# Kernel tuning notes

Measured on AMD Instinct MI355X. Metric: run time of the kernel, lower is better.

Reference implementation:

```python
import jax, jax.numpy as jnp
import numpy as np

DIM = 256
HEADS = 8
DIM_HEAD = 64
INNER = HEADS * DIM_HEAD  # 512
B, H, W = 4, 128, 128


def setup_inputs() -> dict:
    key = jax.random.key(0)
    ks = jax.random.split(key, 7)
    x = jax.random.normal(ks[0], (B, DIM, H, W), dtype=jnp.float32)
    context = jax.random.normal(ks[1], (B, DIM, H, W), dtype=jnp.float32)
    # weights stored as (in, out) so projection is x @ W
    s_in = 1.0 / np.sqrt(DIM)
    s_inner = 1.0 / np.sqrt(INNER)
    Wq = jax.random.uniform(ks[2], (DIM, INNER), jnp.float32, -s_in, s_in)
    Wk = jax.random.uniform(ks[3], (DIM, INNER), jnp.float32, -s_in, s_in)
    Wv = jax.random.uniform(ks[4], (DIM, INNER), jnp.float32, -s_in, s_in)
    Wo = jax.random.uniform(ks[5], (INNER, DIM), jnp.float32, -s_inner, s_inner)
    bo = jax.random.uniform(ks[6], (DIM,), jnp.float32, -s_inner, s_inner)
    return {"x": x, "context": context, "Wq": Wq, "Wk": Wk, "Wv": Wv, "Wo": Wo, "bo": bo}


def reference(x, context, Wq, Wk, Wv, Wo, bo):
    b, c, h, w = x.shape
    n = h * w
    x_flat = x.reshape(b, c, n).transpose(0, 2, 1)          # b n c
    ctx_flat = context.reshape(b, c, n).transpose(0, 2, 1)  # b n c
    # projections; split heads: b n (h d) -> b h n d
    def heads(t):
        return t.reshape(b, n, HEADS, DIM_HEAD).transpose(0, 2, 1, 3)
    q = heads(x_flat @ Wq)
    k = heads(ctx_flat @ Wk)
    v = heads(ctx_flat @ Wv)
    # column-wise softmax over token dim n (axis=-2). NOTE: original module
    # defines scale but never applies it, so we faithfully omit it.
    k = jax.nn.softmax(k, axis=-2)
    cm = jnp.einsum('bhnd,bhne->bhde', k, v)   # small d x e context matrix
    out = jnp.einsum('bhnd,bhde->bhne', q, cm)  # b h n e
    out = out.transpose(0, 2, 1, 3).reshape(b, n, INNER)
    out = out @ Wo + bo
    out = out.transpose(0, 2, 1).reshape(b, c, h, w)
    return x + out
```

## Files before the change

### kernel.cpp

```cpp
#include <hip/hip_runtime.h>

typedef unsigned short u16;
typedef u16   u16x4  __attribute__((ext_vector_type(4)));
typedef u16   u16x8  __attribute__((ext_vector_type(8)));
typedef __bf16 bf16x8 __attribute__((ext_vector_type(8)));
typedef float f32x4  __attribute__((ext_vector_type(4)));

constexpr int BATCH  = 4;
constexpr int CDIM   = 256;
constexpr int NTOK   = 16384;
constexpr int INNERD = 512;

__device__ __forceinline__ u16 f2b(float f) {
  return __builtin_bit_cast(u16, (__bf16)f);
}
__device__ __forceinline__ float b2f(u16 b) {
  return (float)__builtin_bit_cast(__bf16, b);
}

__device__ __forceinline__ void async_ld16(const u16* g, u16* l) {
  __builtin_amdgcn_global_load_lds(
      (const __attribute__((address_space(1))) void*)g,
      (__attribute__((address_space(3))) void*)l, 16, 0, 0);
}

constexpr int ZERO_N = BATCH * 8 * 64 * 64 + BATCH * INNERD;
__global__ __launch_bounds__(256) void prep(
    const float* __restrict__ x, const float* __restrict__ ctx,
    const float* __restrict__ Wk, const float* __restrict__ Wv,
    u16* __restrict__ xt, u16* __restrict__ ct,
    u16* __restrict__ kt, u16* __restrict__ vt,
    float* __restrict__ zbuf) {
  __shared__ float tile[64][33];
  int id = blockIdx.x;
  if (id < 16384) {
    int bx = id & 511, by = (id >> 9) & 3, zb = id >> 11;
    int b = zb >> 1;
    const float* src = (zb & 1) ? ctx : x;
    u16* dst = (zb & 1) ? ct : xt;
    src += (size_t)b * CDIM * NTOK;
    dst += (size_t)b * NTOK * CDIM;
    int n0 = bx * 32, c0 = by * 64;
    int tx = threadIdx.x & 31, ty = threadIdx.x >> 5;
#pragma unroll
    for (int i = 0; i < 64; i += 8)
      tile[ty + i][tx] = src[(size_t)(c0 + ty + i) * NTOK + n0 + tx];
    __syncthreads();
    int nl = threadIdx.x >> 3;
    int cl = (threadIdx.x & 7) * 8;
    u16x8 o;
#pragma unroll
    for (int j = 0; j < 8; j++) o[j] = f2b(tile[cl + j][nl]);
    *(u16x8*)&dst[(size_t)(n0 + nl) * CDIM + c0 + cl] = o;
  } else if (id < 16640) {
    int idw = id - 16384;
    int bx = idw & 15, by = (idw >> 4) & 7, bz = idw >> 7;
    float (*t2)[33] = (float(*)[33])tile;
    const float* src = bz == 0 ? Wk : Wv;
    u16* dst = bz == 0 ? kt : vt;
    int i0 = bx * 32, c0 = by * 32;
    int tx = threadIdx.x & 31, ty = threadIdx.x >> 5;
#pragma unroll
    for (int r = 0; r < 32; r += 8)
      t2[ty + r][tx] = src[(size_t)(c0 + ty + r) * INNERD + i0 + tx];
    __syncthreads();
#pragma unroll
    for (int r = 0; r < 32; r += 8)
      dst[(size_t)(i0 + ty + r) * CDIM + c0 + tx] = f2b(t2[tx][ty + r]);
  } else {
    int i = (id - 16640) * 256 + threadIdx.x;
    if (i < ZERO_N) zbuf[i] = 0.0f;
  }
}

__global__ __launch_bounds__(256, 2) void proj_ctx(
    const u16* __restrict__ Wkt, const u16* __restrict__ Wvt,
    const u16* __restrict__ ctx_bt, float* __restrict__ cm, float* __restrict__ ksum) {
  int id = blockIdx.x;
  int swz = (id & 7) * 64 + (id >> 3);
  int ig = swz & 3, nc = (swz >> 2) & 31, b = swz >> 7;
  int i0 = ig * 128;
  const u16* Bt = ctx_bt + (size_t)b * NTOK * CDIM;

  __shared__ __align__(16) u16 smem[32768];
  u16* Ek = smem + 16384;
  u16* Vt = smem;

  int tid = threadIdx.x, wave = tid >> 6, lane = tid & 63;
  int wm = (wave >> 1) * 64, wn = (wave & 1) * 64;
  int quad = lane >> 4, l16 = lane & 15;
  int sr = lane >> 2, sc = (lane & 3) * 8;

  int hl = wave >> 1, dblk = (wave & 1) * 32;

  u16x8 ov;
#pragma unroll
  for (int t = 0; t < 8; t++) ov[t] = 0x3f80;
  const bf16x8 ones = __builtin_bit_cast(bf16x8, ov);

  f32x4 acc_cm[2][4];
  f32x4 accS[2];
#pragma unroll
  for (int i = 0; i < 2; i++) {
    accS[i] = (f32x4)(0.0f);
#pragma unroll
    for (int j = 0; j < 4; j++) acc_cm[i][j] = (f32x4)(0.0f);
  }

  auto stage = [&](int p, int kv, int ks, int n0) {
    int k0 = ks * 32;
    const u16* Asrc = kv ? Wvt : Wkt;
#pragma unroll
    for (int j = 0; j < 4; j++) {
      int c = wave * 4 + j;
      if (c < 8) {
        int row = c * 16 + sr;
        async_ld16(&Asrc[(size_t)(i0 + row) * CDIM + k0 + sc], &smem[p * 8192 + c * 512]);
      } else {
        int cb = c - 8, row = cb * 16 + sr;
        async_ld16(&Bt[(size_t)(n0 + row) * CDIM + k0 + sc], &smem[p * 8192 + 4096 + cb * 512]);
      }
    }
  };

  for (int nt = 0; nt < 4; nt++) {
    int n0 = nc * 512 + nt * 128;
    __syncthreads();
    stage(0, 0, 0, n0);
    __syncthreads();

    f32x4 acc[4][4];
#pragma unroll
    for (int i = 0; i < 4; i++)
#pragma unroll
      for (int j = 0; j < 4; j++) acc[i][j] = (f32x4)(0.0f);

#pragma unroll 2
    for (int s = 0; s < 16; s++) {
      int p = s & 1;
      if (s < 15) { int s1 = s + 1; stage(p ^ 1, s1 >> 3, s1 & 7, n0); }
      const u16* As = &smem[p * 8192];
      const u16* Bs = &smem[p * 8192 + 4096];
      bf16x8 af[4], bfr[4];
#pragma unroll
      for (int m = 0; m < 4; m++)
        af[m] = __builtin_bit_cast(bf16x8, *(const u16x8*)&As[(wm + m * 16 + l16) * 32 + quad * 8]);
#pragma unroll
      for (int e = 0; e < 4; e++)
        bfr[e] = __builtin_bit_cast(bf16x8, *(const u16x8*)&Bs[(wn + e * 16 + l16) * 32 + quad * 8]);
#pragma unroll
      for (int e = 0; e < 4; e++)
#pragma unroll
        for (int m = 0; m < 4; m++)
          acc[e][m] = __builtin_amdgcn_mfma_f32_16x16x32_bf16(bfr[e], af[m], acc[e][m], 0, 0, 0);

      if (s == 7) {
#pragma unroll
        for (int e = 0; e < 4; e++) {
          int nl0 = wn + e * 16 + quad * 4;
#pragma unroll
          for (int m = 0; m < 4; m++) {
            int row = wm + m * 16 + l16;
            u16x4 ok;
#pragma unroll
            for (int r = 0; r < 4; r++) ok[r] = f2b(__expf(acc[e][m][r]));
            unsigned byt = (unsigned)(row * 256 + nl0 * 2) ^ ((unsigned)(row & 7) << 4);
            *(u16x4*)((char*)Ek + byt) = ok;
            acc[e][m] = (f32x4)(0.0f);
          }
        }
      }
      __syncthreads();
    }
#pragma unroll
    for (int e = 0; e < 4; e++) {
      int nl0 = wn + e * 16 + quad * 4;
#pragma unroll
      for (int m = 0; m < 4; m++) {
        int row = wm + m * 16 + l16;
        u16x4 ovv;
#pragma unroll
        for (int r = 0; r < 4; r++) ovv[r] = f2b(acc[e][m][r]);
        unsigned byt = (unsigned)(row * 256 + nl0 * 2) ^ ((unsigned)(row & 7) << 4);
        *(u16x4*)((char*)Vt + byt) = ovv;
      }
    }
    __syncthreads();
#pragma unroll
    for (int kk = 0; kk < 128; kk += 32) {
      int ko = kk + quad * 8;
      bf16x8 ea[2], vb[4];
#pragma unroll
      for (int m2 = 0; m2 < 2; m2++) {
        int row = hl * 64 + dblk + m2 * 16 + l16;
        unsigned byt = (unsigned)(row * 256 + ko * 2) ^ ((unsigned)(row & 7) << 4);
        ea[m2] = __builtin_bit_cast(bf16x8, *(const u16x8*)((char*)Ek + byt));
      }
#pragma unroll
      for (int e2 = 0; e2 < 4; e2++) {
        int row = hl * 64 + e2 * 16 + l16;
        unsigned byt = (unsigned)(row * 256 + ko * 2) ^ ((unsigned)(row & 7) << 4);
        vb[e2] = __builtin_bit_cast(bf16x8, *(const u16x8*)((char*)Vt + byt));
      }
#pragma unroll
      for (int m2 = 0; m2 < 2; m2++) {
        accS[m2] = __builtin_amdgcn_mfma_f32_16x16x32_bf16(ea[m2], ones, accS[m2], 0, 0, 0);
#pragma unroll
        for (int e2 = 0; e2 < 4; e2++)
          acc_cm[m2][e2] = __builtin_amdgcn_mfma_f32_16x16x32_bf16(ea[m2], vb[e2], acc_cm[m2][e2], 0, 0, 0);
      }
    }
  }
  int h = ig * 2 + hl;
  float* cmp = cm + (size_t)(b * 8 + h) * 64 * 64;
#pragma unroll
  for (int m2 = 0; m2 < 2; m2++)
#pragma unroll
    for (int e2 = 0; e2 < 4; e2++)
#pragma unroll
      for (int r = 0; r < 4; r++) {
        int d = dblk + m2 * 16 + quad * 4 + r;
        int e = e2 * 16 + l16;
        atomicAdd(&cmp[d * 64 + e], acc_cm[m2][e2][r]);
      }
  if (l16 == 0) {
#pragma unroll
    for (int m2 = 0; m2 < 2; m2++)
#pragma unroll
      for (int r = 0; r < 4; r++) {
        int d = dblk + m2 * 16 + quad * 4 + r;
        atomicAdd(&ksum[(size_t)b * INNERD + h * 64 + d], accS[m2][r]);
      }
  }
}

__global__ __launch_bounds__(256) void weff_k(
    const float* __restrict__ cm, const float* __restrict__ Wo,
    const float* __restrict__ ksum, float* __restrict__ weff) {
  int bi = blockIdx.x;
  int b = bi >> 9, i = bi & 511, h = i >> 6, d = i & 63;
  const float* cmr = cm + ((size_t)(b * 8 + h) * 64 + d) * 64;
  __shared__ float cs[64];
  if (threadIdx.x < 64) cs[threadIdx.x] = cmr[threadIdx.x];
  __syncthreads();
  float inv = 1.0f / ksum[(size_t)b * INNERD + i];
  int c = threadIdx.x;
  float s = 0.0f;
#pragma unroll 8
  for (int e = 0; e < 64; e++) s += cs[e] * Wo[(size_t)(h * 64 + e) * CDIM + c];
  weff[(size_t)bi * CDIM + c] = s * inv;
}

__global__ __launch_bounds__(256) void gt_k(
    const float* __restrict__ weff, const float* __restrict__ Wq, u16* __restrict__ Gt) {
  int bc = blockIdx.x;
  int b = bc >> 8, c = bc & 255;
  __shared__ float ws[512];
  for (int j = threadIdx.x; j < 512; j += 256)
    ws[j] = weff[((size_t)b * 512 + j) * CDIM + c];
  __syncthreads();
  int cp = threadIdx.x;
  float s = 0.0f;
#pragma unroll 8
  for (int i = 0; i < 512; i += 4) {
    f32x4 q = *(const f32x4*)&Wq[(size_t)cp * INNERD + i];
    s += ws[i] * q[0] + ws[i + 1] * q[1] + ws[i + 2] * q[2] + ws[i + 3] * q[3];
  }
  Gt[(size_t)bc * CDIM + cp] = f2b(s);
}

__global__ __launch_bounds__(256) void final_gemm(
    const u16* __restrict__ Gt, const u16* __restrict__ x_bt,
    const float* __restrict__ x, const float* __restrict__ bo,
    float* __restrict__ out) {
  int id = blockIdx.x;
  int swz = (id & 7) * 128 + (id >> 3);
  int bx = swz & 1, by = (swz >> 1) & 127, b = swz >> 8;
  const u16* A  = Gt + (size_t)b * CDIM * CDIM;
  const u16* Bt = x_bt + (size_t)b * NTOK * CDIM;
  const float* xb = x + (size_t)b * CDIM * NTOK;
  float* ob = out + (size_t)b * CDIM * NTOK;
  int i0 = bx * 128;
  int n0 = by * 128;

  __shared__ __align__(16) u16 smem2[16384];

  int tid = threadIdx.x;
  int wave = tid >> 6, lane = tid & 63;
  int wm = (wave >> 1) * 64, wn = (wave & 1) * 64;
  int quad = lane >> 4, l16 = lane & 15;
  int sr = lane >> 2, sc = (lane & 3) * 8;

  auto stage = [&](int p, int ks) {
    int k0 = ks * 32;
#pragma unroll
    for (int j = 0; j < 4; j++) {
      int c = wave * 4 + j;
      if (c < 8) {
        int row = c * 16 + sr;
        async_ld16(&A[(size_t)(i0 + row) * CDIM + k0 + sc], &smem2[p * 8192 + c * 512]);
      } else {
        int cb = c - 8, row = cb * 16 + sr;
        async_ld16(&Bt[(size_t)(n0 + row) * CDIM + k0 + sc], &smem2[p * 8192 + 4096 + cb * 512]);
      }
    }
  };

  f32x4 acc[4][4];
#pragma unroll
  for (int i = 0; i < 4; i++)
#pragma unroll
    for (int j = 0; j < 4; j++) acc[i][j] = (f32x4)(0.0f);

  stage(0, 0);
  __syncthreads();
#pragma unroll 2
  for (int s = 0; s < 8; s++) {
    int p = s & 1;
    if (s < 7) stage(p ^ 1, s + 1);
    const u16* As = &smem2[p * 8192];
    const u16* Bs = &smem2[p * 8192 + 4096];
    bf16x8 af[4], bfr[4];
#pragma unroll
    for (int m = 0; m < 4; m++)
      af[m] = __builtin_bit_cast(bf16x8, *(const u16x8*)&As[(wm + m * 16 + l16) * 32 + quad * 8]);
#pragma unroll
    for (int e = 0; e < 4; e++)
      bfr[e] = __builtin_bit_cast(bf16x8, *(const u16x8*)&Bs[(wn + e * 16 + l16) * 32 + quad * 8]);
#pragma unroll
    for (int e = 0; e < 4; e++)
#pragma unroll
      for (int m = 0; m < 4; m++)
        acc[e][m] = __builtin_amdgcn_mfma_f32_16x16x32_bf16(bfr[e], af[m], acc[e][m], 0, 0, 0);
    if (s < 7) __syncthreads();
  }
#pragma unroll
  for (int e = 0; e < 4; e++) {
    int nb = n0 + wn + e * 16 + quad * 4;
#pragma unroll
    for (int m = 0; m < 4; m++) {
      int c = i0 + wm + m * 16 + l16;
      f32x4 xv = *(const f32x4*)&xb[(size_t)c * NTOK + nb];
      f32x4 r;
      float bc = bo[c];
#pragma unroll
      for (int t = 0; t < 4; t++) r[t] = acc[e][m][t] + xv[t] + bc;
      *(f32x4*)&ob[(size_t)c * NTOK + nb] = r;
    }
  }
}

extern "C" void kernel_launch(void* const* d_in, const int* in_sizes, int n_in,
                              void* d_out, int out_size, void* d_ws, size_t ws_size,
                              hipStream_t stream) {
  const float* x   = (const float*)d_in[0];
  const float* ctx = (const float*)d_in[1];
  const float* Wq  = (const float*)d_in[2];
  const float* Wk  = (const float*)d_in[3];
  const float* Wv  = (const float*)d_in[4];
  const float* Wo  = (const float*)d_in[5];
  const float* bo  = (const float*)d_in[6];
  float* out = (float*)d_out;

  char* ws = (char*)d_ws;
  u16* ctx_bt = (u16*)ws;  ws += (size_t)BATCH * NTOK * CDIM * 2;
  u16* x_bt   = (u16*)ws;  ws += (size_t)BATCH * NTOK * CDIM * 2;
  u16* Wk_t   = (u16*)ws;  ws += (size_t)INNERD * CDIM * 2;
  u16* Wv_t   = (u16*)ws;  ws += (size_t)INNERD * CDIM * 2;
  float* cm   = (float*)ws; ws += (size_t)BATCH * 8 * 64 * 64 * 4;
  float* ksum = (float*)ws; ws += (size_t)BATCH * INNERD * 4;
  float* weff = (float*)ws; ws += (size_t)BATCH * INNERD * CDIM * 4;
  u16* Gt     = (u16*)ws;  ws += (size_t)BATCH * CDIM * CDIM * 2;

  prep<<<dim3(17160), 256, 0, stream>>>(x, ctx, Wk, Wv, x_bt, ctx_bt,
                                        Wk_t, Wv_t, cm );
  proj_ctx<<<dim3(512), 256, 0, stream>>>(Wk_t, Wv_t, ctx_bt, cm, ksum);
  weff_k<<<BATCH * INNERD, 256, 0, stream>>>(cm, Wo, ksum, weff);
  gt_k<<<BATCH * CDIM, 256, 0, stream>>>(weff, Wq, Gt);
  final_gemm<<<dim3(1024), 256, 0, stream>>>(Gt, x_bt, x, bo, out);
}
```

Before: 342.5 us.

## Compute Gt with a bf16 MFMA tiled GEMM using pre-converted Wq and transposed weff

```diff
diff --git a/kernel.cpp b/kernel.cpp
--- a/kernel.cpp
+++ b/kernel.cpp
@@ -28,8 +28,9 @@
 __global__ __launch_bounds__(256) void prep(
     const float* __restrict__ x, const float* __restrict__ ctx,
     const float* __restrict__ Wk, const float* __restrict__ Wv,
+    const float* __restrict__ Wq,
     u16* __restrict__ xt, u16* __restrict__ ct,
-    u16* __restrict__ kt, u16* __restrict__ vt,
+    u16* __restrict__ kt, u16* __restrict__ vt, u16* __restrict__ qc,
     float* __restrict__ zbuf) {
   __shared__ float tile[64][33];
   int id = blockIdx.x;
@@ -67,8 +68,16 @@
 #pragma unroll
     for (int r = 0; r < 32; r += 8)
       dst[(size_t)(i0 + ty + r) * CDIM + c0 + tx] = f2b(t2[tx][ty + r]);
+  } else if (id < 16704) {
+    size_t off = (size_t)(id - 16640) * 2048 + threadIdx.x * 8;
+    f32x4 a = *(const f32x4*)&Wq[off];
+    f32x4 c = *(const f32x4*)&Wq[off + 4];
+    u16x8 o;
+#pragma unroll
+    for (int j = 0; j < 4; j++) { o[j] = f2b(a[j]); o[j + 4] = f2b(c[j]); }
+    *(u16x8*)&qc[off] = o;
   } else {
-    int i = (id - 16640) * 256 + threadIdx.x;
+    int i = (id - 16704) * 256 + threadIdx.x;
     if (i < ZERO_N) zbuf[i] = 0.0f;
   }
 }
@@ -236,7 +245,7 @@
 
 __global__ __launch_bounds__(256) void weff_k(
     const float* __restrict__ cm, const float* __restrict__ Wo,
-    const float* __restrict__ ksum, float* __restrict__ weff) {
+    const float* __restrict__ ksum, u16* __restrict__ weff_t) {
   int bi = blockIdx.x;
   int b = bi >> 9, i = bi & 511, h = i >> 6, d = i & 63;
   const float* cmr = cm + ((size_t)(b * 8 + h) * 64 + d) * 64;
@@ -248,25 +257,81 @@
   float s = 0.0f;
 #pragma unroll 8
   for (int e = 0; e < 64; e++) s += cs[e] * Wo[(size_t)(h * 64 + e) * CDIM + c];
-  weff[(size_t)bi * CDIM + c] = s * inv;
+  weff_t[((size_t)b * CDIM + c) * INNERD + i] = f2b(s * inv);
 }
 
 __global__ __launch_bounds__(256) void gt_k(
-    const float* __restrict__ weff, const float* __restrict__ Wq, u16* __restrict__ Gt) {
-  int bc = blockIdx.x;
-  int b = bc >> 8, c = bc & 255;
-  __shared__ float ws[512];
-  for (int j = threadIdx.x; j < 512; j += 256)
-    ws[j] = weff[((size_t)b * 512 + j) * CDIM + c];
+    const u16* __restrict__ weff_t, const u16* __restrict__ Wqc, u16* __restrict__ Gt) {
+  int id = blockIdx.x;
+  int bx = id & 1, by = (id >> 1) & 1, b = id >> 2;
+  const u16* A  = weff_t + (size_t)b * CDIM * INNERD;
+  const u16* Bt = Wqc;
+  int i0 = bx * 128;
+  int n0 = by * 128;
+
+  __shared__ __align__(16) u16 smem3[16384];
+
+  int tid = threadIdx.x;
+  int wave = tid >> 6, lane = tid & 63;
+  int wm = (wave >> 1) * 64, wn = (wave & 1) * 64;
+  int quad = lane >> 4, l16 = lane & 15;
+  int sr = lane >> 2, sc = (lane & 3) * 8;
+
+  auto stage = [&](int p, int ks) {
+    int k0 = ks * 32;
+#pragma unroll
+    for (int j = 0; j < 4; j++) {
+      int c = wave * 4 + j;
+      if (c < 8) {
+        int row = c * 16 + sr;
+        async_ld16(&A[(size_t)(i0 + row) * INNERD + k0 + sc], &smem3[p * 8192 + c * 512]);
+      } else {
+        int cb = c - 8, row = cb * 16 + sr;
+        async_ld16(&Bt[(size_t)(n0 + row) * INNERD + k0 + sc], &smem3[p * 8192 + 4096 + cb * 512]);
+      }
+    }
+  };
+
+  f32x4 acc[4][4];
+#pragma unroll
+  for (int i = 0; i < 4; i++)
+#pragma unroll
+    for (int j = 0; j < 4; j++) acc[i][j] = (f32x4)(0.0f);
+
+  stage(0, 0);
   __syncthreads();
-  int cp = threadIdx.x;
-  float s = 0.0f;
-#pragma unroll 8
-  for (int i = 0; i < 512; i += 4) {
-    f32x4 q = *(const f32x4*)&Wq[(size_t)cp * INNERD + i];
-    s += ws[i] * q[0] + ws[i + 1] * q[1] + ws[i + 2] * q[2] + ws[i + 3] * q[3];
-  }
-  Gt[(size_t)bc * CDIM + cp] = f2b(s);
+#pragma unroll 2
+  for (int s = 0; s < 16; s++) {
+    int p = s & 1;
+    if (s < 15) stage(p ^ 1, s + 1);
+    const u16* As = &smem3[p * 8192];
+    const u16* Bs = &smem3[p * 8192 + 4096];
+    bf16x8 af[4], bfr[4];
+#pragma unroll
+    for (int m = 0; m < 4; m++)
+      af[m] = __builtin_bit_cast(bf16x8, *(const u16x8*)&As[(wm + m * 16 + l16) * 32 + quad * 8]);
+#pragma unroll
+    for (int e = 0; e < 4; e++)
+      bfr[e] = __builtin_bit_cast(bf16x8, *(const u16x8*)&Bs[(wn + e * 16 + l16) * 32 + quad * 8]);
+#pragma unroll
+    for (int e = 0; e < 4; e++)
+#pragma unroll
+      for (int m = 0; m < 4; m++)
+        acc[e][m] = __builtin_amdgcn_mfma_f32_16x16x32_bf16(bfr[e], af[m], acc[e][m], 0, 0, 0);
+    if (s < 15) __syncthreads();
+  }
+#pragma unroll
+  for (int e = 0; e < 4; e++) {
+    int nb = n0 + wn + e * 16 + quad * 4;
+#pragma unroll
+    for (int m = 0; m < 4; m++) {
+      int c = i0 + wm + m * 16 + l16;
+      u16x4 o;
+#pragma unroll
+      for (int r = 0; r < 4; r++) o[r] = f2b(acc[e][m][r]);
+      *(u16x4*)&Gt[((size_t)b * CDIM + c) * CDIM + nb] = o;
+    }
+  }
 }
 
 __global__ __launch_bounds__(256) void final_gemm(
@@ -367,15 +432,16 @@
   u16* x_bt   = (u16*)ws;  ws += (size_t)BATCH * NTOK * CDIM * 2;
   u16* Wk_t   = (u16*)ws;  ws += (size_t)INNERD * CDIM * 2;
   u16* Wv_t   = (u16*)ws;  ws += (size_t)INNERD * CDIM * 2;
+  u16* Wqc    = (u16*)ws;  ws += (size_t)CDIM * INNERD * 2;
   float* cm   = (float*)ws; ws += (size_t)BATCH * 8 * 64 * 64 * 4;
   float* ksum = (float*)ws; ws += (size_t)BATCH * INNERD * 4;
-  float* weff = (float*)ws; ws += (size_t)BATCH * INNERD * CDIM * 4;
+  u16* weff_t = (u16*)ws;  ws += (size_t)BATCH * CDIM * INNERD * 2;
   u16* Gt     = (u16*)ws;  ws += (size_t)BATCH * CDIM * CDIM * 2;
 
-  prep<<<dim3(17160), 256, 0, stream>>>(x, ctx, Wk, Wv, x_bt, ctx_bt,
-                                        Wk_t, Wv_t, cm );
+  prep<<<dim3(17224), 256, 0, stream>>>(x, ctx, Wk, Wv, Wq, x_bt, ctx_bt,
+                                        Wk_t, Wv_t, Wqc, cm );
   proj_ctx<<<dim3(512), 256, 0, stream>>>(Wk_t, Wv_t, ctx_bt, cm, ksum);
-  weff_k<<<BATCH * INNERD, 256, 0, stream>>>(cm, Wo, ksum, weff);
-  gt_k<<<BATCH * CDIM, 256, 0, stream>>>(weff, Wq, Gt);
+  weff_k<<<BATCH * INNERD, 256, 0, stream>>>(cm, Wo, ksum, weff_t);
+  gt_k<<<dim3(16), 256, 0, stream>>>(weff_t, Wqc, Gt);
   final_gemm<<<dim3(1024), 256, 0, stream>>>(Gt, x_bt, x, bo, out);
 }
```

Result: faster. 297.6 us (-13.1%).
